# Kernel tuning notes

Measured on AMD Instinct MI355X. Metric: run time of the kernel, lower is better.

The kernel has to match this reference:

```python
import jax, jax.numpy as jnp
import numpy as np

TOTAL_BITS = 16
FRAC_BITS = 8
SCALE = 2.0 ** FRAC_BITS
QMIN = -(2.0 ** (TOTAL_BITS - 1)) / SCALE
QMAX = (2.0 ** (TOTAL_BITS - 1) - 1) / SCALE


def quant(x):
    # fixed-point quantize: round to frac_bits, clamp to total_bits range (STE grad)
    q = jnp.clip(jnp.round(x * SCALE) / SCALE, QMIN, QMAX)
    return x + jax.lax.stop_gradient(q - x)


def hard_sigmoid(x):
    return jnp.clip(x / 6.0 + 0.5, 0.0, 1.0)


def hard_tanh(x):
    return jnp.clip(x, -1.0, 1.0)


def setup_inputs() -> dict:
    key = jax.random.key(0)
    ks = jax.random.split(key, 7)
    B, T, I, H, O = 256, 512, 128, 256, 1
    return {
        "x": jax.random.normal(ks[0], (B, T, I), jnp.float32),
        "w_ih": jax.random.normal(ks[1], (4 * H, I), jnp.float32) * 0.05,
        "w_hh": jax.random.normal(ks[2], (4 * H, H), jnp.float32) * 0.05,
        "b_ih": jax.random.normal(ks[3], (4 * H,), jnp.float32) * 0.05,
        "b_hh": jax.random.normal(ks[4], (4 * H,), jnp.float32) * 0.05,
        "w_lin": jax.random.normal(ks[5], (O, H), jnp.float32) * 0.05,
        "b_lin": jax.random.normal(ks[6], (O,), jnp.float32) * 0.05,
    }


def reference(x, w_ih, w_hh, b_ih, b_hh, w_lin, b_lin):
    B, T, I = x.shape
    H = w_hh.shape[1]
    xq = quant(x)
    w_ih_q, w_hh_q = quant(w_ih), quant(w_hh)
    b_ih_q, b_hh_q = quant(b_ih), quant(b_hh)
    # input projection for all timesteps at once: [B,T,4H]
    gi = quant(jnp.einsum("bti,gi->btg", xq, w_ih_q) + b_ih_q)

    def step(carry, gi_t):
        h, c = carry
        gh = quant(h @ w_hh_q.T + b_hh_q)
        g = quant(gi_t + gh)
        i_g, f_g, c_g, o_g = jnp.split(g, 4, axis=-1)
        i_g = quant(hard_sigmoid(i_g))
        f_g = quant(hard_sigmoid(f_g))
        c_g = quant(hard_tanh(c_g))
        o_g = quant(hard_sigmoid(o_g))
        c_new = quant(quant(f_g * c) + quant(i_g * c_g))
        h_new = quant(o_g * quant(hard_tanh(c_new)))
        return (h_new, c_new), None

    h0 = jnp.zeros((B, H), x.dtype)
    c0 = jnp.zeros((B, H), x.dtype)
    (h_last, _), _ = jax.lax.scan(step, (h0, c0), jnp.swapaxes(gi, 0, 1))
    # x[:, -1] of the LSTM output == h_last; fixed-point linear head
    return quant(h_last @ quant(w_lin).T + quant(b_lin))
```

## Files before the change

### kernel.cpp

```cpp
#include <hip/hip_runtime.h>
#include <stdint.h>
#include <stddef.h>

typedef int i32x4 __attribute__((ext_vector_type(4)));
typedef int i32x2 __attribute__((ext_vector_type(2)));

#define WS_WFRAG   0u
#define WS_WIH     262144u
#define WS_BIASHH  393216u
#define WS_BIASIH  397312u
#define WS_WLIN    401408u
#define WS_BLIN    402432u
#define WS_HSTATE  409600u
#define WS_CSTATE  540672u
#define WS_GI      1048576u

#define MFMA_I8(a,b,c) __builtin_amdgcn_mfma_i32_16x16x64_i8(a,b,c,0,0,0)
#define RHE8(x) ((((x) + 127) + (((x) >> 8) & 1)) >> 8)

#define BAR() do { asm volatile("s_waitcnt lgkmcnt(0)" ::: "memory"); \
                   __builtin_amdgcn_s_barrier(); } while (0)

__device__ __forceinline__ float clamp3(float x, float lo, float hi) {
    return __builtin_amdgcn_fmed3f(x, lo, hi);
}
__device__ __forceinline__ float q16f(float x) {
    return clamp3(__builtin_rintf(x * 256.0f), -32768.0f, 32767.0f);
}
__device__ __forceinline__ int iclamp(int v, int lo, int hi) {
    return v < lo ? lo : (v > hi ? hi : v);
}

__global__ void prep_kernel(const float* __restrict__ wih, const float* __restrict__ whh,
                            const float* __restrict__ bih, const float* __restrict__ bhh,
                            const float* __restrict__ wlin, const float* __restrict__ blin,
                            uint8_t* __restrict__ ws) {
    int tid = blockIdx.x * blockDim.x + threadIdx.x;
    {
        int p = tid;
        int j = p & 15, lane = (p >> 4) & 63, ks = (p >> 10) & 3, t8 = (p >> 12) & 7, w = (p >> 15) & 7;
        int row = (t8 >> 1) * 256 + w * 32 + (t8 & 1) * 16 + (lane & 15);
        int k = ks * 64 + (lane >> 4) * 16 + j;
        int v = (int)q16f(whh[row * 256 + k]);
        v = iclamp(v, -127, 127);
        ((int8_t*)(ws + WS_WFRAG))[p] = (int8_t)v;
    }
    if (tid < 131072) {
        int gcol = tid >> 7, k = tid & 127;
        int v = (int)q16f(wih[gcol * 128 + k]);
        v = iclamp(v, -127, 127);
        ((int8_t*)(ws + WS_WIH))[tid] = (int8_t)v;
    }
    if (tid < 1024) {
        ((int*)(ws + WS_BIASHH))[tid] = ((int)q16f(bhh[tid])) * 256;
        ((int*)(ws + WS_BIASIH))[tid] = ((int)q16f(bih[tid])) * 256;
    }
    if (tid < 256) ((int*)(ws + WS_WLIN))[tid] = (int)q16f(wlin[tid]);
    if (tid == 0)  ((int*)(ws + WS_BLIN))[0]   = (int)q16f(blin[0]);
}

__launch_bounds__(512, 2)
__global__ void gi_kernel(const float* __restrict__ x, uint8_t* __restrict__ ws, int t0) {
    __shared__ uint8_t xa[2048], xb[2048];
    int tid = threadIdx.x;
    int wgr = blockIdx.x;
    int tl  = blockIdx.y;
    int t   = t0 + tl;
    {
        int row = tid >> 5, c4 = (tid & 31) * 4;
        int b = wgr * 16 + row;
        const float4 xv = *(const float4*)(x + ((size_t)b * 512 + t) * 128 + c4);
        int v0 = (int)q16f(xv.x), v1 = (int)q16f(xv.y), v2 = (int)q16f(xv.z), v3 = (int)q16f(xv.w);
        uint32_t da = ((uint32_t)((v0 >> 7) & 255)) | ((uint32_t)((v1 >> 7) & 255) << 8) |
                      ((uint32_t)((v2 >> 7) & 255) << 16) | ((uint32_t)((v3 >> 7) & 255) << 24);
        uint32_t db = ((uint32_t)(v0 & 127)) | ((uint32_t)(v1 & 127) << 8) |
                      ((uint32_t)(v2 & 127) << 16) | ((uint32_t)(v3 & 127) << 24);
        int addr = row * 128 + (((c4 >> 4) ^ (row & 7)) * 16) + (c4 & 15);
        *(uint32_t*)(xa + addr) = da;
        *(uint32_t*)(xb + addr) = db;
    }
    __syncthreads();
    int wid = tid >> 6, lane = tid & 63, lr = lane & 15, lg = lane >> 4;
    const uint8_t* wq = ws + WS_WIH;
    i32x4 af[8][2];
#pragma unroll
    for (int mt = 0; mt < 8; ++mt) {
        int gcol = (mt >> 1) * 256 + wid * 32 + (mt & 1) * 16 + lr;
#pragma unroll
        for (int kt = 0; kt < 2; ++kt)
            af[mt][kt] = *(const i32x4*)(wq + gcol * 128 + kt * 64 + lg * 16);
    }
    i32x4 bha[2], bhb[2];
#pragma unroll
    for (int kt = 0; kt < 2; ++kt) {
        int addr = lr * 128 + ((((kt * 4) + lg) ^ (lr & 7)) * 16);
        bha[kt] = *(const i32x4*)(xa + addr);
        bhb[kt] = *(const i32x4*)(xb + addr);
    }
    i32x4 acch[8], accl[8];
    const int* bi = (const int*)(ws + WS_BIASIH);
#pragma unroll
    for (int mt = 0; mt < 8; ++mt) {
        i32x4 z = {0, 0, 0, 0};
        int gb = (mt >> 1) * 256 + wid * 32 + (mt & 1) * 16 + lg * 4;
        i32x4 bc = *(const i32x4*)(bi + gb);
        acch[mt] = MFMA_I8(af[mt][0], bha[0], z);
        accl[mt] = MFMA_I8(af[mt][0], bhb[0], bc);
        acch[mt] = MFMA_I8(af[mt][1], bha[1], acch[mt]);
        accl[mt] = MFMA_I8(af[mt][1], bhb[1], accl[mt]);
    }
    int gq[8][4];
#pragma unroll
    for (int mt = 0; mt < 8; ++mt)
#pragma unroll
        for (int rr = 0; rr < 4; ++rr) {
            int v = acch[mt][rr] * 128 + accl[mt][rr];
            gq[mt][rr] = iclamp(RHE8(v), -32768, 32767);
        }
    unsigned wb = (unsigned)(wgr * 8 + (lr >> 1));
#pragma unroll
    for (int mm2 = 0; mm2 < 2; ++mm2)
#pragma unroll
        for (int rr2 = 0; rr2 < 4; ++rr2) {
            i32x2 outv;
            outv[0] = (gq[mm2][rr2] & 0xFFFF)     | (gq[2 + mm2][rr2] << 16);
            outv[1] = (gq[4 + mm2][rr2] & 0xFFFF) | (gq[6 + mm2][rr2] << 16);
            int lane_d = (rr2 & 1) | ((lr & 1) << 1) | (mm2 << 2) | ((rr2 >> 1) << 3) | (lg << 4);
            *(i32x2*)(ws + WS_GI + (size_t)tl * 524288u +
                      (size_t)((wb * 8u + (unsigned)wid) * 64u + (unsigned)lane_d) * 8u) = outv;
        }
}

__launch_bounds__(512, 2)
__global__ void recur_kernel(uint8_t* __restrict__ ws, float* __restrict__ out, int t0, int cs) {
    __shared__ __align__(16) uint8_t hbuf[2][1024];
    __shared__ unsigned short lut[1544];
    __shared__ long long redl[8][2];
    int tid = threadIdx.x, w = tid >> 6, lane = tid & 63;
    int wb = blockIdx.x;
    int cp = lane & 1;
    int cb = (lane >> 1) & 1;
    int mm = (lane >> 2) & 1;
    int X  = (lane >> 3) & 1;
    int sg = lane >> 4;
    uint8_t* hb0 = &hbuf[0][0];

    for (int u = tid; u < 1537; u += 512) {
        double y = ((double)(u - 768) / 256.0) / 6.0 + 0.5;
        y = y < 0.0 ? 0.0 : (y > 1.0 ? 1.0 : y);
        lut[u] = (unsigned short)(int)__builtin_rint(y * 256.0);
    }

    i32x4 wf[8][4];
#pragma unroll
    for (int t8 = 0; t8 < 8; ++t8)
#pragma unroll
        for (int ks = 0; ks < 4; ++ks)
            wf[t8][ks] = *(const i32x4*)(ws + WS_WFRAG + (((unsigned)(w * 8 + t8) * 4 + ks) << 10) + lane * 16);

    int addrB[4];
#pragma unroll
    for (int ks = 0; ks < 4; ++ks)
        addrB[ks] = (cb * 2 + cp) * 256 + ((ks * 64 + sg * 16) ^ (cp << 6) ^ (cb << 5));

    int k_own = w * 32 + mm * 16 + sg * 4 + 2 * X + cp;
    int addrWa = cb * 512 + (k_own ^ (cb << 5));
    int addrWb = cb * 512 + 256 + (k_own ^ 64 ^ (cb << 5));
    int biasP[4], wlv;
    {
        const int* bhh256 = (const int*)(ws + WS_BIASHH);
#pragma unroll
        for (int G = 0; G < 4; ++G)
            biasP[G] = bhh256[G * 256 + k_own] + (G == 2 ? 0 : 768 * 256);
        wlv = ((const int*)(ws + WS_WLIN))[k_own];
    }
    size_t gioff = (size_t)((unsigned)wb * 8u + (unsigned)w) * 512u + (unsigned)lane * 8u;

    uint8_t* hst = ws + WS_HSTATE + (unsigned)wb * 1024u;
    int* cst = (int*)(ws + WS_CSTATE) + (unsigned)wb * 512u + (unsigned)tid;

    int c_;
    if (t0 == 0) {
        c_ = 0;
        if (tid < 256) *(uint32_t*)(hb0 + tid * 4) = 0u;
    } else {
        c_ = *cst;
        if (tid < 256) *(uint32_t*)(hb0 + tid * 4) = *(const uint32_t*)(hst + tid * 4);
    }
    i32x2 gcur = *(const i32x2*)(ws + WS_GI + gioff);
    i32x2 gnx;
    __syncthreads();

    int hl_ = 0;
    const i32x4 zerov = {0, 0, 0, 0};

#define GIV(GUSE, G) ((G & 1) ? (GUSE[G >> 1] >> 16) : ((GUSE[G >> 1] << 16) >> 16))
#define SLOT(G, OUTV)                                                                  \
    {                                                                                  \
        int u0 = X ? acc[2 * G][2]     : acc[2 * G][0];                                \
        int u1 = X ? acc[2 * G][3]     : acc[2 * G][1];                                \
        int v0 = X ? acc[2 * G + 1][2] : acc[2 * G + 1][0];                            \
        int v1 = X ? acc[2 * G + 1][3] : acc[2 * G + 1][1];                            \
        int w0 = mm ? v0 : u0;                                                         \
        int w1 = mm ? v1 : u1;                                                         \
        int own = cp ? w1 : w0;                                                        \
        int snd = cp ? w0 : w1;                                                        \
        int z = __builtin_amdgcn_ds_swizzle(snd, 0x41F);                               \
        int d = cp ? ((z << 2) + own) : ((own << 2) + z);                              \
        OUTV = RHE8(d + biasP[G]);                                                     \
    }
#define STEP(PP, GUSE, GPRE, TPRE)                                                     \
    {                                                                                  \
        GPRE = *(const i32x2*)(ws + WS_GI + (size_t)(TPRE) * 524288u + gioff);         \
        i32x4 acc[8];                                                                  \
        _Pragma("unroll")                                                              \
        for (int ks = 0; ks < 4; ++ks) {                                               \
            i32x4 bf = *(const i32x4*)(hb0 + (PP) * 1024 + addrB[ks]);                 \
            _Pragma("unroll")                                                          \
            for (int t8 = 0; t8 < 8; ++t8)                                             \
                acc[t8] = (ks == 0) ? MFMA_I8(wf[t8][0], bf, zerov)                    \
                                    : MFMA_I8(wf[t8][ks], bf, acc[t8]);                \
        }                                                                              \
        int g0, g1, g2, g3;                                                            \
        SLOT(0, g0) SLOT(1, g1) SLOT(2, g2) SLOT(3, g3)                                \
        int gate0 = (int)lut[iclamp(g0 + GIV(GUSE, 0), 0, 1536)];                      \
        int gate1 = (int)lut[iclamp(g1 + GIV(GUSE, 1), 0, 1536)];                      \
        int gate2 = iclamp(g2 + GIV(GUSE, 2), -256, 256);                              \
        int gate3 = (int)lut[iclamp(g3 + GIV(GUSE, 3), 0, 1536)];                      \
        int fcq = RHE8(__mul24(gate1, c_));                                            \
        int icq = RHE8(__mul24(gate0, gate2));                                         \
        int cn  = iclamp(fcq + icq, -32768, 32767);                                    \
        c_ = cn;                                                                       \
        int th = iclamp(cn, -256, 256);                                                \
        int hq = RHE8(__mul24(gate3, th));                                             \
        *(int8_t*)(hb0 + ((PP) ^ 1) * 1024 + addrWa) = (int8_t)(hq >> 2);              \
        *(int8_t*)(hb0 + ((PP) ^ 1) * 1024 + addrWb) = (int8_t)(hq & 3);               \
        hl_ = hq;                                                                      \
        BAR();                                                                         \
    }

    for (int tl = 0; tl < cs; tl += 2) {
        int tn2 = (tl + 2 < cs) ? tl + 2 : 0;
        STEP(0, gcur, gnx, tl + 1)
        STEP(1, gnx, gcur, tn2)
    }
#undef STEP
#undef SLOT
#undef GIV

    if (tid < 256) *(uint32_t*)(hst + tid * 4) = *(const uint32_t*)(hb0 + tid * 4);
    *cst = c_;

    if (t0 + cs == 512) {
        long long s = (long long)hl_ * (long long)wlv;
        s += __shfl_xor(s, 1);
        s += __shfl_xor(s, 4);
        s += __shfl_xor(s, 8);
        s += __shfl_xor(s, 16);
        s += __shfl_xor(s, 32);
        if ((lane & 61) == 0) redl[w][cb] = s;
        __syncthreads();
        if (tid < 2) {
            long long tot = 0;
#pragma unroll
            for (int ww = 0; ww < 8; ++ww) tot += redl[ww][tid];
            tot += 256LL * (long long)((const int*)(ws + WS_BLIN))[0];
            long long q = ((tot + 127) + ((tot >> 8) & 1)) >> 8;
            q = q < -32768 ? -32768 : (q > 32767 ? 32767 : q);
            out[wb * 2 + tid] = (float)q * 0.00390625f;
        }
    }
}

extern "C" void kernel_launch(void* const* d_in, const int* in_sizes, int n_in,
                              void* d_out, int out_size, void* d_ws, size_t ws_size,
                              hipStream_t stream) {
    const float* x    = (const float*)d_in[0];
    const float* wih  = (const float*)d_in[1];
    const float* whh  = (const float*)d_in[2];
    const float* bih  = (const float*)d_in[3];
    const float* bhh  = (const float*)d_in[4];
    const float* wlin = (const float*)d_in[5];
    const float* blin = (const float*)d_in[6];
    float* out = (float*)d_out;
    uint8_t* ws = (uint8_t*)d_ws;

    prep_kernel<<<512, 512, 0, stream>>>(wih, whh, bih, bhh, wlin, blin, ws);

    int cs = 512;
    while ((size_t)WS_GI + (size_t)cs * 524288u > ws_size && cs > 8) cs >>= 1;

    for (int t0 = 0; t0 < 512; t0 += cs) {
        gi_kernel<<<dim3(16, cs), 512, 0, stream>>>(x, ws, t0);
        recur_kernel<<<128, 512, 0, stream>>>(ws, out, t0, cs);
    }
}
```

Baseline: 596.4 us.

## Split recurrence to one batch row per block and double block count

Each recurrent block now handles a single batch row instead of two, so the launch uses 256 blocks instead of 128. Lanes that previously split work between two batch rows now split the four gates between lane pairs, exchanging gate values with swizzles. The gate-input layout in the projection kernel is changed to match. This spreads the serial recurrence over more compute units at the cost of extra cross-lane shuffles and duplicated weight-fragment loads per block.

```diff
diff --git a/kernel.cpp b/kernel.cpp
--- a/kernel.cpp
+++ b/kernel.cpp
@@ -13,7 +13,7 @@
 #define WS_BLIN    402432u
 #define WS_HSTATE  409600u
 #define WS_CSTATE  540672u
-#define WS_GI      1048576u
+#define WS_GI      1064960u
 
 #define MFMA_I8(a,b,c) __builtin_amdgcn_mfma_i32_16x16x64_i8(a,b,c,0,0,0)
 #define RHE8(x) ((((x) + 127) + (((x) >> 8) & 1)) >> 8)
@@ -117,32 +117,32 @@
             int v = acch[mt][rr] * 128 + accl[mt][rr];
             gq[mt][rr] = iclamp(RHE8(v), -32768, 32767);
         }
-    unsigned wb = (unsigned)(wgr * 8 + (lr >> 1));
+    unsigned batch = (unsigned)(wgr * 16 + lr);
 #pragma unroll
     for (int mm2 = 0; mm2 < 2; ++mm2)
 #pragma unroll
         for (int rr2 = 0; rr2 < 4; ++rr2) {
             i32x2 outv;
-            outv[0] = (gq[mm2][rr2] & 0xFFFF)     | (gq[2 + mm2][rr2] << 16);
-            outv[1] = (gq[4 + mm2][rr2] & 0xFFFF) | (gq[6 + mm2][rr2] << 16);
-            int lane_d = (rr2 & 1) | ((lr & 1) << 1) | (mm2 << 2) | ((rr2 >> 1) << 3) | (lg << 4);
+            outv[0] = (gq[mm2][rr2] & 0xFFFF)     | (gq[4 + mm2][rr2] << 16);
+            outv[1] = (gq[2 + mm2][rr2] & 0xFFFF) | (gq[6 + mm2][rr2] << 16);
+            int Lp = ((rr2 & 1) << 1) | (mm2 << 2) | ((rr2 >> 1) << 3) | (lg << 4);
             *(i32x2*)(ws + WS_GI + (size_t)tl * 524288u +
-                      (size_t)((wb * 8u + (unsigned)wid) * 64u + (unsigned)lane_d) * 8u) = outv;
+                      (size_t)((batch * 8u + (unsigned)wid) * 64u + (unsigned)Lp) * 4u) = outv;
         }
 }
 
 __launch_bounds__(512, 2)
 __global__ void recur_kernel(uint8_t* __restrict__ ws, float* __restrict__ out, int t0, int cs) {
-    __shared__ __align__(16) uint8_t hbuf[2][1024];
+    __shared__ __align__(16) uint8_t hbuf[2][512];
     __shared__ unsigned short lut[1544];
-    __shared__ long long redl[8][2];
+    __shared__ long long redl[8];
     int tid = threadIdx.x, w = tid >> 6, lane = tid & 63;
     int wb = blockIdx.x;
-    int cp = lane & 1;
-    int cb = (lane >> 1) & 1;
-    int mm = (lane >> 2) & 1;
-    int X  = (lane >> 3) & 1;
-    int sg = lane >> 4;
+    int gsel = lane & 1;
+    int cp   = (lane >> 1) & 1;
+    int mm   = (lane >> 2) & 1;
+    int X    = (lane >> 3) & 1;
+    int sg   = lane >> 4;
     uint8_t* hb0 = &hbuf[0][0];
 
     for (int u = tid; u < 1537; u += 512) {
@@ -161,80 +161,94 @@
     int addrB[4];
 #pragma unroll
     for (int ks = 0; ks < 4; ++ks)
-        addrB[ks] = (cb * 2 + cp) * 256 + ((ks * 64 + sg * 16) ^ (cp << 6) ^ (cb << 5));
+        addrB[ks] = cp * 256 + ks * 64 + sg * 16;
 
     int k_own = w * 32 + mm * 16 + sg * 4 + 2 * X + cp;
-    int addrWa = cb * 512 + (k_own ^ (cb << 5));
-    int addrWb = cb * 512 + 256 + (k_own ^ 64 ^ (cb << 5));
-    int biasP[4], wlv;
+    int addrW = (gsel ? 256 : 0) + k_own;
+    int biasP[2], wlv;
     {
         const int* bhh256 = (const int*)(ws + WS_BIASHH);
-#pragma unroll
-        for (int G = 0; G < 4; ++G)
-            biasP[G] = bhh256[G * 256 + k_own] + (G == 2 ? 0 : 768 * 256);
+        int G0 = gsel, G1 = gsel + 2;
+        biasP[0] = bhh256[G0 * 256 + k_own] + 768 * 256;
+        biasP[1] = bhh256[G1 * 256 + k_own] + (G1 == 2 ? 0 : 768 * 256);
         wlv = ((const int*)(ws + WS_WLIN))[k_own];
     }
-    size_t gioff = (size_t)((unsigned)wb * 8u + (unsigned)w) * 512u + (unsigned)lane * 8u;
-
-    uint8_t* hst = ws + WS_HSTATE + (unsigned)wb * 1024u;
+    size_t gioff = (size_t)((unsigned)wb * 8u + (unsigned)w) * 256u + (unsigned)lane * 4u;
+
+    uint8_t* hst = ws + WS_HSTATE + (unsigned)wb * 512u;
     int* cst = (int*)(ws + WS_CSTATE) + (unsigned)wb * 512u + (unsigned)tid;
 
     int c_;
     if (t0 == 0) {
         c_ = 0;
-        if (tid < 256) *(uint32_t*)(hb0 + tid * 4) = 0u;
+        if (tid < 128) *(uint32_t*)(hb0 + tid * 4) = 0u;
     } else {
         c_ = *cst;
-        if (tid < 256) *(uint32_t*)(hb0 + tid * 4) = *(const uint32_t*)(hst + tid * 4);
-    }
-    i32x2 gcur = *(const i32x2*)(ws + WS_GI + gioff);
-    i32x2 gnx;
+        if (tid < 128) *(uint32_t*)(hb0 + tid * 4) = *(const uint32_t*)(hst + tid * 4);
+    }
+    int gcur = *(const int*)(ws + WS_GI + gioff);
+    int gnx;
     __syncthreads();
 
     int hl_ = 0;
     const i32x4 zerov = {0, 0, 0, 0};
 
-#define GIV(GUSE, G) ((G & 1) ? (GUSE[G >> 1] >> 16) : ((GUSE[G >> 1] << 16) >> 16))
-#define SLOT(G, OUTV)                                                                  \
+#define PLANEPAIR(T0, T1, T2, T3, U, V)                                                \
+    int U, V;                                                                          \
     {                                                                                  \
-        int u0 = X ? acc[2 * G][2]     : acc[2 * G][0];                                \
-        int u1 = X ? acc[2 * G][3]     : acc[2 * G][1];                                \
-        int v0 = X ? acc[2 * G + 1][2] : acc[2 * G + 1][0];                            \
-        int v1 = X ? acc[2 * G + 1][3] : acc[2 * G + 1][1];                            \
-        int w0 = mm ? v0 : u0;                                                         \
-        int w1 = mm ? v1 : u1;                                                         \
-        int own = cp ? w1 : w0;                                                        \
-        int snd = cp ? w0 : w1;                                                        \
-        int z = __builtin_amdgcn_ds_swizzle(snd, 0x41F);                               \
-        int d = cp ? ((z << 2) + own) : ((own << 2) + z);                              \
-        OUTV = RHE8(d + biasP[G]);                                                     \
+        int ua = X ? acc[T0][2] : acc[T0][0], va = X ? acc[T0][3] : acc[T0][1];        \
+        int ub = X ? acc[T1][2] : acc[T1][0], vb = X ? acc[T1][3] : acc[T1][1];        \
+        int uc = X ? acc[T2][2] : acc[T2][0], vc = X ? acc[T2][3] : acc[T2][1];        \
+        int ud = X ? acc[T3][2] : acc[T3][0], vd = X ? acc[T3][3] : acc[T3][1];        \
+        int u0 = mm ? ub : ua, v0 = mm ? vb : va;                                      \
+        int u1 = mm ? ud : uc, v1 = mm ? vd : vc;                                      \
+        U = gsel ? u1 : u0;                                                            \
+        V = gsel ? v1 : v0;                                                            \
+    }
+#define SLOT(U, V, BIAS, OUTG)                                                         \
+    int OUTG;                                                                          \
+    {                                                                                  \
+        int own = cp ? V : U;                                                          \
+        int snd = cp ? U : V;                                                          \
+        int z = __builtin_amdgcn_ds_swizzle(snd, 0x081F);                              \
+        int hi = cp ? z : own;                                                         \
+        int lo = cp ? own : z;                                                         \
+        OUTG = RHE8(hi * 4 + lo + (BIAS));                                             \
     }
 #define STEP(PP, GUSE, GPRE, TPRE)                                                     \
     {                                                                                  \
-        GPRE = *(const i32x2*)(ws + WS_GI + (size_t)(TPRE) * 524288u + gioff);         \
+        GPRE = *(const int*)(ws + WS_GI + (size_t)(TPRE) * 524288u + gioff);           \
         i32x4 acc[8];                                                                  \
         _Pragma("unroll")                                                              \
         for (int ks = 0; ks < 4; ++ks) {                                               \
-            i32x4 bf = *(const i32x4*)(hb0 + (PP) * 1024 + addrB[ks]);                 \
+            i32x4 bf = *(const i32x4*)(hb0 + (PP) * 512 + addrB[ks]);                  \
             _Pragma("unroll")                                                          \
             for (int t8 = 0; t8 < 8; ++t8)                                             \
                 acc[t8] = (ks == 0) ? MFMA_I8(wf[t8][0], bf, zerov)                    \
                                     : MFMA_I8(wf[t8][ks], bf, acc[t8]);                \
         }                                                                              \
-        int g0, g1, g2, g3;                                                            \
-        SLOT(0, g0) SLOT(1, g1) SLOT(2, g2) SLOT(3, g3)                                \
-        int gate0 = (int)lut[iclamp(g0 + GIV(GUSE, 0), 0, 1536)];                      \
-        int gate1 = (int)lut[iclamp(g1 + GIV(GUSE, 1), 0, 1536)];                      \
-        int gate2 = iclamp(g2 + GIV(GUSE, 2), -256, 256);                              \
-        int gate3 = (int)lut[iclamp(g3 + GIV(GUSE, 3), 0, 1536)];                      \
-        int fcq = RHE8(__mul24(gate1, c_));                                            \
-        int icq = RHE8(__mul24(gate0, gate2));                                         \
+        PLANEPAIR(0, 1, 2, 3, uA, vA)                                                  \
+        PLANEPAIR(4, 5, 6, 7, uB, vB)                                                  \
+        SLOT(uA, vA, biasP[0], gA)                                                     \
+        SLOT(uB, vB, biasP[1], gB)                                                     \
+        int givlo = ((GUSE) << 16) >> 16, givhi = (GUSE) >> 16;                        \
+        int first = (int)lut[iclamp(gA + givlo, 0, 1536)];     \
+        int lutB  = (int)lut[iclamp(gB + givhi, 0, 1536)];                             \
+        int clpB  = iclamp(gB - 768 * 0 + givhi, -256, 256);   \
+        int second = gsel ? lutB : clpB;                       \
+        int z1 = __builtin_amdgcn_ds_swizzle(first, 0x041F);                           \
+        int z2 = __builtin_amdgcn_ds_swizzle(second, 0x041F);                          \
+        int i_g = gsel ? z1 : first;                                                   \
+        int f_g = gsel ? first : z1;                                                   \
+        int c_g = gsel ? z2 : second;                                                  \
+        int o_g = gsel ? second : z2;                                                  \
+        int fcq = RHE8(__mul24(f_g, c_));                                              \
+        int icq = RHE8(__mul24(i_g, c_g));                                             \
         int cn  = iclamp(fcq + icq, -32768, 32767);                                    \
         c_ = cn;                                                                       \
         int th = iclamp(cn, -256, 256);                                                \
-        int hq = RHE8(__mul24(gate3, th));                                             \
-        *(int8_t*)(hb0 + ((PP) ^ 1) * 1024 + addrWa) = (int8_t)(hq >> 2);              \
-        *(int8_t*)(hb0 + ((PP) ^ 1) * 1024 + addrWb) = (int8_t)(hq & 3);               \
+        int hq = RHE8(__mul24(o_g, th));                                               \
+        *(int8_t*)(hb0 + ((PP) ^ 1) * 512 + addrW) = (int8_t)(gsel ? (hq & 3) : (hq >> 2)); \
         hl_ = hq;                                                                      \
         BAR();                                                                         \
     }
@@ -246,28 +260,29 @@
     }
 #undef STEP
 #undef SLOT
-#undef GIV
-
-    if (tid < 256) *(uint32_t*)(hst + tid * 4) = *(const uint32_t*)(hb0 + tid * 4);
+#undef PLANEPAIR
+
+    if (tid < 128) *(uint32_t*)(hst + tid * 4) = *(const uint32_t*)(hb0 + tid * 4);
     *cst = c_;
 
     if (t0 + cs == 512) {
-        long long s = (long long)hl_ * (long long)wlv;
+        long long s = gsel ? 0LL : (long long)hl_ * (long long)wlv;
         s += __shfl_xor(s, 1);
+        s += __shfl_xor(s, 2);
         s += __shfl_xor(s, 4);
         s += __shfl_xor(s, 8);
         s += __shfl_xor(s, 16);
         s += __shfl_xor(s, 32);
-        if ((lane & 61) == 0) redl[w][cb] = s;
+        if (lane == 0) redl[w] = s;
         __syncthreads();
-        if (tid < 2) {
+        if (tid == 0) {
             long long tot = 0;
 #pragma unroll
-            for (int ww = 0; ww < 8; ++ww) tot += redl[ww][tid];
+            for (int ww = 0; ww < 8; ++ww) tot += redl[ww];
             tot += 256LL * (long long)((const int*)(ws + WS_BLIN))[0];
             long long q = ((tot + 127) + ((tot >> 8) & 1)) >> 8;
             q = q < -32768 ? -32768 : (q > 32767 ? 32767 : q);
-            out[wb * 2 + tid] = (float)q * 0.00390625f;
+            out[wb] = (float)q * 0.00390625f;
         }
     }
 }
@@ -292,6 +307,6 @@
 
     for (int t0 = 0; t0 < 512; t0 += cs) {
         gi_kernel<<<dim3(16, cs), 512, 0, stream>>>(x, ws, t0);
-        recur_kernel<<<128, 512, 0, stream>>>(ws, out, t0, cs);
-    }
-}
+        recur_kernel<<<256, 512, 0, stream>>>(ws, out, t0, cs);
+    }
+}
```

After: 638.7 us. 1.07x slower.
